# Kernel tuning notes

Hardware: AMD Instinct MI355X
Metric: run time of the kernel (lower is better)

Reference implementation:

```python
import jax, jax.numpy as jnp
import numpy as np


def setup_inputs() -> dict:
    key = jax.random.key(0)
    k1, k2 = jax.random.split(key)
    center = jax.random.normal(k1, (4096,), dtype=jnp.float32)
    error = jax.random.normal(k2, (8192, 4096), dtype=jnp.float32) * 0.01
    return {"center": center, "error": error}


def reference(center, error):
    # Zonotope ReLU abstract transformer.
    center_orig_shape = center.shape
    error_orig_shape = error.shape
    c = center.reshape(-1)                      # (d,)
    e = error.reshape(error.shape[0], -1)       # (n_error, d)
    n_error, d = e.shape

    apt = jnp.sum(jnp.abs(e), axis=0)           # (d,) interval radius
    ub = c + apt
    lb = c - apt

    cross = (ub > 0) & (lb < 0)                 # unstable neurons
    act = lb >= 0                               # stably active
    # dead (ub <= 0): slope = 0, mu = 0 -> center/error zeroed

    denom = jnp.where(cross, ub - lb, jnp.float32(1.0))
    slope = jnp.where(cross, ub / denom, jnp.float32(0.0))
    mu = jnp.where(cross, -slope * lb * jnp.float32(0.5), jnp.float32(0.0))

    new_center = jnp.where(act, c, slope * c + mu)          # (d,)
    col_scale = jnp.where(act, jnp.float32(1.0), slope)     # (d,)
    top = e * col_scale[None, :]                             # (n_error, d)
    # One fresh error term per crossing neuron; padded to d rows (diagonal),
    # zero rows where the neuron is not crossing (static output shape).
    bottom = jnp.diag(mu)                                    # (d, d)
    new_error = jnp.concatenate([top, bottom], axis=0)       # (n_error + d, d)

    new_center = new_center.reshape(center_orig_shape)
    new_error = new_error.reshape((n_error + d,) + error_orig_shape[1:])
    return new_center, new_error
```

## Files before the change

kernel.cpp:

```cpp
#include <hip/hip_runtime.h>

#define D        4096
#define NERR     8192
#define ROWCH    64
#define RPC      (NERR / ROWCH)
#define D4       (D / 4)

typedef float f32x4 __attribute__((ext_vector_type(4)));

__global__ void k_colsum_partial(const f32x4* __restrict__ e4,
                                 f32x4* __restrict__ part4) {
    const int t     = threadIdx.x;
    const int cb    = blockIdx.x & 3;
    const int chunk = blockIdx.x >> 2;
    const int col4  = cb * 256 + t;
    const f32x4* p = e4 + (size_t)chunk * RPC * D4 + col4;

    f32x4 acc = (f32x4)(0.f, 0.f, 0.f, 0.f);
    #pragma unroll 8
    for (int r = 0; r < RPC; ++r) {
        f32x4 v = p[(size_t)r * D4];
        acc.x += fabsf(v.x);
        acc.y += fabsf(v.y);
        acc.z += fabsf(v.z);
        acc.w += fabsf(v.w);
    }
    part4[chunk * D4 + col4] = acc;
}

__global__ void k_finalize_cols(const float* __restrict__ part,
                                const float* __restrict__ center,
                                float* __restrict__ out_center,
                                float* __restrict__ col_scale,
                                float* __restrict__ mu_arr) {
    const int col = blockIdx.x * 256 + threadIdx.x;
    float apt = 0.f;
    #pragma unroll 8
    for (int k = 0; k < ROWCH; ++k) apt += part[k * D + col];

    const float c  = center[col];
    const float ub = c + apt;
    const float lb = c - apt;
    const bool cross = (ub > 0.f) && (lb < 0.f);
    const bool act   = (lb >= 0.f);

    const float denom = cross ? (ub - lb) : 1.f;
    const float slope = cross ? (ub / denom) : 0.f;
    const float mu    = cross ? (-slope * lb * 0.5f) : 0.f;

    out_center[col] = act ? c : (slope * c + mu);
    col_scale[col]  = act ? 1.f : slope;
    mu_arr[col]     = mu;
}

__global__ void k_scale_top(const f32x4* __restrict__ e4,
                            const f32x4* __restrict__ cs4,
                            f32x4* __restrict__ out4) {
    const int n4     = NERR * D4;
    const int stride = gridDim.x * blockDim.x;
    const int tid    = blockIdx.x * blockDim.x + threadIdx.x;
    const f32x4 s    = cs4[tid & (D4 - 1)];
    for (int i = tid; i < n4; i += stride) {
        f32x4 v = __builtin_nontemporal_load(&e4[i]);
        v *= s;
        __builtin_nontemporal_store(v, &out4[i]);
    }
}

__global__ void k_write_bottom(const float* __restrict__ mu_arr,
                               f32x4* __restrict__ out4) {
    const int n4     = D * D4;
    const int stride = gridDim.x * blockDim.x;
    const int tid    = blockIdx.x * blockDim.x + threadIdx.x;
    const int j4     = tid & (D4 - 1);
    for (int i = tid; i < n4; i += stride) {
        const int row = i >> 10;
        f32x4 v = (f32x4)(0.f, 0.f, 0.f, 0.f);
        if (j4 == (row >> 2)) {
            v[row & 3] = mu_arr[row];
        }
        __builtin_nontemporal_store(v, &out4[i]);
    }
}

extern "C" void kernel_launch(void* const* d_in, const int* in_sizes, int n_in,
                              void* d_out, int out_size, void* d_ws, size_t ws_size,
                              hipStream_t stream) {
    const float* center = (const float*)d_in[0];
    const float* error  = (const float*)d_in[1];
    float* out = (float*)d_out;
    float* ws  = (float*)d_ws;

    float* part      = ws;
    float* col_scale = ws + (size_t)ROWCH * D;
    float* mu_arr    = col_scale + D;

    float* out_center = out;
    float* out_top    = out + D;
    float* out_bottom = out + (size_t)D + (size_t)NERR * D;

    k_colsum_partial<<<ROWCH * 4, 256, 0, stream>>>(
        (const f32x4*)error, (f32x4*)part);
    k_finalize_cols<<<D / 256, 256, 0, stream>>>(
        part, center, out_center, col_scale, mu_arr);
    k_scale_top<<<2048, 256, 0, stream>>>(
        (const f32x4*)error, (const f32x4*)col_scale, (f32x4*)out_top);
    k_write_bottom<<<2048, 256, 0, stream>>>(
        mu_arr, (f32x4*)out_bottom);
}
```

Baseline: 87.70 us.

## Overlap bottom zero-fill with column reduction and scatter diagonal from finalize

The separate bottom-matrix kernel is removed. Extra blocks in the first-phase kernel zero the 64MB diagonal block while the other blocks compute column abs-sums, so the write-only work overlaps the read-bound reduction. The finalize kernel writes mu directly onto the diagonal, and it now reduces 128 chunks per column with wavefront shuffles over a transposed partials layout. This drops one launch and the extra pass over the bottom region, but adds a strided transposed store of partials and a write-after-write ordering dependency between the kernels.

```diff
diff --git a/kernel.cpp b/kernel.cpp
--- a/kernel.cpp
+++ b/kernel.cpp
@@ -2,60 +2,85 @@
 
 #define D        4096
 #define NERR     8192
-#define ROWCH    64
-#define RPC      (NERR / ROWCH)
 #define D4       (D / 4)
+#define CHUNKS   128
+#define RPC      (NERR / CHUNKS)
 
 typedef float f32x4 __attribute__((ext_vector_type(4)));
 
-__global__ void k_colsum_partial(const f32x4* __restrict__ e4,
-                                 f32x4* __restrict__ part4) {
-    const int t     = threadIdx.x;
-    const int cb    = blockIdx.x & 3;
-    const int chunk = blockIdx.x >> 2;
-    const int col4  = cb * 256 + t;
-    const f32x4* p = e4 + (size_t)chunk * RPC * D4 + col4;
+__global__ __launch_bounds__(256) void k_phase1(const f32x4* __restrict__ e4,
+                                                float* __restrict__ part_t,
+                                                f32x4* __restrict__ bot4) {
+    const int t   = threadIdx.x;
+    const int bid = blockIdx.x;
+    if (bid < 512) {
+        const int cb    = bid & 3;
+        const int chunk = bid >> 2;
+        const int col4  = cb * 256 + t;
+        const f32x4* p  = e4 + (size_t)chunk * RPC * D4 + col4;
 
-    f32x4 acc = (f32x4)(0.f, 0.f, 0.f, 0.f);
-    #pragma unroll 8
-    for (int r = 0; r < RPC; ++r) {
-        f32x4 v = p[(size_t)r * D4];
-        acc.x += fabsf(v.x);
-        acc.y += fabsf(v.y);
-        acc.z += fabsf(v.z);
-        acc.w += fabsf(v.w);
+        f32x4 acc = (f32x4)(0.f, 0.f, 0.f, 0.f);
+        #pragma unroll 8
+        for (int r = 0; r < RPC; ++r) {
+            f32x4 v = p[(size_t)r * D4];
+            acc.x += fabsf(v.x);
+            acc.y += fabsf(v.y);
+            acc.z += fabsf(v.z);
+            acc.w += fabsf(v.w);
+        }
+        const size_t colbase = (size_t)col4 * 4;
+        part_t[(colbase + 0) * CHUNKS + chunk] = acc.x;
+        part_t[(colbase + 1) * CHUNKS + chunk] = acc.y;
+        part_t[(colbase + 2) * CHUNKS + chunk] = acc.z;
+        part_t[(colbase + 3) * CHUNKS + chunk] = acc.w;
+    } else {
+        const int fb = bid - 512;
+        const size_t base = (size_t)fb * 8192;
+        const f32x4 z = (f32x4)(0.f, 0.f, 0.f, 0.f);
+        #pragma unroll
+        for (int j = 0; j < 32; ++j)
+            __builtin_nontemporal_store(z, &bot4[base + (size_t)j * 256 + t]);
     }
-    part4[chunk * D4 + col4] = acc;
 }
 
-__global__ void k_finalize_cols(const float* __restrict__ part,
-                                const float* __restrict__ center,
-                                float* __restrict__ out_center,
-                                float* __restrict__ col_scale,
-                                float* __restrict__ mu_arr) {
-    const int col = blockIdx.x * 256 + threadIdx.x;
-    float apt = 0.f;
-    #pragma unroll 8
-    for (int k = 0; k < ROWCH; ++k) apt += part[k * D + col];
+__global__ __launch_bounds__(256) void k_finalize(const float* __restrict__ part_t,
+                                                  const float* __restrict__ center,
+                                                  float* __restrict__ out_center,
+                                                  float* __restrict__ col_scale,
+                                                  float* __restrict__ out_bottom) {
+    const int w    = threadIdx.x >> 6;
+    const int lane = threadIdx.x & 63;
+    const int colbase = blockIdx.x * 16 + w * 4;
 
-    const float c  = center[col];
-    const float ub = c + apt;
-    const float lb = c - apt;
-    const bool cross = (ub > 0.f) && (lb < 0.f);
-    const bool act   = (lb >= 0.f);
+    #pragma unroll
+    for (int u = 0; u < 4; ++u) {
+        const int col  = colbase + u;
+        const float* p = part_t + (size_t)col * CHUNKS;
+        float s = p[lane] + p[lane + 64];
+        #pragma unroll
+        for (int off = 32; off > 0; off >>= 1)
+            s += __shfl_xor(s, off, 64);
+        if (lane == 0) {
+            const float apt = s;
+            const float c   = center[col];
+            const float ub  = c + apt;
+            const float lb  = c - apt;
+            const bool cross = (ub > 0.f) && (lb < 0.f);
+            const bool act   = (lb >= 0.f);
+            const float denom = cross ? (ub - lb) : 1.f;
+            const float slope = cross ? (ub / denom) : 0.f;
+            const float mu    = cross ? (-slope * lb * 0.5f) : 0.f;
 
-    const float denom = cross ? (ub - lb) : 1.f;
-    const float slope = cross ? (ub / denom) : 0.f;
-    const float mu    = cross ? (-slope * lb * 0.5f) : 0.f;
-
-    out_center[col] = act ? c : (slope * c + mu);
-    col_scale[col]  = act ? 1.f : slope;
-    mu_arr[col]     = mu;
+            out_center[col] = act ? c : (slope * c + mu);
+            col_scale[col]  = act ? 1.f : slope;
+            out_bottom[(size_t)col * (D + 1)] = mu;
+        }
+    }
 }
 
-__global__ void k_scale_top(const f32x4* __restrict__ e4,
-                            const f32x4* __restrict__ cs4,
-                            f32x4* __restrict__ out4) {
+__global__ __launch_bounds__(256) void k_scale_top(const f32x4* __restrict__ e4,
+                                                   const f32x4* __restrict__ cs4,
+                                                   f32x4* __restrict__ out4) {
     const int n4     = NERR * D4;
     const int stride = gridDim.x * blockDim.x;
     const int tid    = blockIdx.x * blockDim.x + threadIdx.x;
@@ -63,22 +88,6 @@
     for (int i = tid; i < n4; i += stride) {
         f32x4 v = __builtin_nontemporal_load(&e4[i]);
         v *= s;
-        __builtin_nontemporal_store(v, &out4[i]);
-    }
-}
-
-__global__ void k_write_bottom(const float* __restrict__ mu_arr,
-                               f32x4* __restrict__ out4) {
-    const int n4     = D * D4;
-    const int stride = gridDim.x * blockDim.x;
-    const int tid    = blockIdx.x * blockDim.x + threadIdx.x;
-    const int j4     = tid & (D4 - 1);
-    for (int i = tid; i < n4; i += stride) {
-        const int row = i >> 10;
-        f32x4 v = (f32x4)(0.f, 0.f, 0.f, 0.f);
-        if (j4 == (row >> 2)) {
-            v[row & 3] = mu_arr[row];
-        }
         __builtin_nontemporal_store(v, &out4[i]);
     }
 }
@@ -91,20 +100,17 @@
     float* out = (float*)d_out;
     float* ws  = (float*)d_ws;
 
-    float* part      = ws;
-    float* col_scale = ws + (size_t)ROWCH * D;
-    float* mu_arr    = col_scale + D;
+    float* part_t    = ws;
+    float* col_scale = ws + (size_t)D * CHUNKS;
 
     float* out_center = out;
     float* out_top    = out + D;
     float* out_bottom = out + (size_t)D + (size_t)NERR * D;
 
-    k_colsum_partial<<<ROWCH * 4, 256, 0, stream>>>(
-        (const f32x4*)error, (f32x4*)part);
-    k_finalize_cols<<<D / 256, 256, 0, stream>>>(
-        part, center, out_center, col_scale, mu_arr);
+    k_phase1<<<1024, 256, 0, stream>>>(
+        (const f32x4*)error, part_t, (f32x4*)out_bottom);
+    k_finalize<<<256, 256, 0, stream>>>(
+        part_t, center, out_center, col_scale, out_bottom);
     k_scale_top<<<2048, 256, 0, stream>>>(
         (const f32x4*)error, (const f32x4*)col_scale, (f32x4*)out_top);
-    k_write_bottom<<<2048, 256, 0, stream>>>(
-        mu_arr, (f32x4*)out_bottom);
 }
```

Result: slower. 90.71 us (+3.4%).
